# Kernel tuning notes

Measured on AMD Instinct MI355X. Metric: run time of the kernel, lower is better.

## Reference

```python
import jax, jax.numpy as jnp
import numpy as np

B, T, DIM = 2, 2048, 1040
H = 16
HD = (DIM - 1) // H  # 64 spatial dims per head; per-head width = HD + 1
EPS = 1e-6


def _rotary_tables(seq_len, dtype):
    inv_freq = 1.0 / (10000.0 ** (jnp.arange(0, HD, 2, dtype=jnp.float32) / (HD - 2 * EPS)))
    t = jnp.arange(seq_len, dtype=jnp.float32)
    freqs = jnp.outer(t, inv_freq)  # [T, HD//2]
    cos = jnp.cos(freqs).astype(dtype)[None, :, None, :]  # [1,T,1,HD//2]
    sin = jnp.sin(freqs).astype(dtype)[None, :, None, :]
    return cos, sin


def _apply_hyp_rotary(x, cos, sin):
    # x: [B,T,H,HD+1]; component 0 is the Lorentz time coordinate
    x_sp = x[..., 1:]
    d = x_sp.shape[-1] // 2
    x1, x2 = x_sp[..., :d], x_sp[..., d:]
    y1 = x1 * cos + x2 * sin
    y2 = -x1 * sin + x2 * cos
    rot = jnp.clip(jnp.concatenate([y1, y2], axis=-1), -1000.0, 1000.0)
    sp_sq = jnp.clip(jnp.sum(rot * rot, axis=-1, keepdims=True), 0.0, 1e6)
    new_x0 = jnp.sqrt(1.0 + sp_sq + EPS)  # re-project onto hyperboloid
    return jnp.concatenate([new_x0, rot], axis=-1)


def setup_inputs() -> dict:
    key = jax.random.key(0)
    kx, kq, kk, kv, kp = jax.random.split(key, 5)
    scale = 0.02  # xavier_normal gain 0.02 in the original
    x = jax.random.normal(kx, (B, T, DIM), dtype=jnp.float32)
    Wq = jax.random.normal(kq, (DIM, DIM), dtype=jnp.float32) * scale
    Wk = jax.random.normal(kk, (DIM, DIM), dtype=jnp.float32) * scale
    Wv = jax.random.normal(kv, (DIM, DIM), dtype=jnp.float32) * scale
    Wp = jax.random.normal(kp, (DIM, DIM), dtype=jnp.float32) * scale
    return {"x": x, "Wq": Wq, "Wk": Wk, "Wv": Wv, "Wp": Wp}


def reference(x, Wq, Wk, Wv, Wp):
    b, t, _ = x.shape
    q = (x @ Wq.T).reshape(b, t, H, HD + 1)
    k = (x @ Wk.T).reshape(b, t, H, HD + 1)
    v = (x @ Wv.T).reshape(b, t, H, HD + 1)
    cos, sin = _rotary_tables(t, x.dtype)
    q = _apply_hyp_rotary(q, cos, sin)
    k = _apply_hyp_rotary(k, cos, sin)
    # Lorentzian inner product scores: -q0*k0 + <q_sp, k_sp>
    spatial = jnp.einsum('bthd,bshd->bhts', q[..., 1:], k[..., 1:])
    lorentz = jnp.einsum('bth,bsh->bhts', q[..., 0], k[..., 0])
    logits = jnp.clip((spatial - lorentz) / (HD ** 0.5), -100.0, 100.0)
    attn = jax.nn.softmax(logits, axis=-1)
    y = jnp.einsum('bhts,bshd->bthd', attn, v).reshape(b, t, DIM)
    return y @ Wp.T
```

## Files before the change

### kernel.cpp

```cpp
#include <hip/hip_runtime.h>
#include <math.h>

#define B_   2
#define T_   2048
#define DIM_ 1040
#define H_   16
#define HD_  64
#define HD1_ 65
#define NELEM (B_*T_*DIM_)

#define KP_   1056
#define NP_   1152
#define NP3_  3456
#define SEGS_ 132
#define MROWS_ (B_*T_)

#define NBH_  (B_*H_)
#define VTR_  72
#define QKW_  96

#define PR_A_ (NP3_*SEGS_)
#define PR_B_ (PR_A_ + MROWS_*SEGS_)
#define PR_C_ (PR_B_ + NBH_*7*256)
#define PR_D_ (PR_C_ + NP_*SEGS_)

typedef __attribute__((ext_vector_type(8))) __bf16 bf16x8;
typedef __attribute__((ext_vector_type(4))) float f32x4;
typedef __attribute__((ext_vector_type(8))) unsigned short ushort8;

static __device__ __forceinline__ unsigned pack_bf16(float lo, float hi) {
    __bf16 a = (__bf16)lo, c = (__bf16)hi;
    unsigned short ua, uc;
    __builtin_memcpy(&ua, &a, 2);
    __builtin_memcpy(&uc, &c, 2);
    return ((unsigned)uc << 16) | ua;
}

static __device__ __forceinline__ float exp2_fast(float x) {
    float r;
    asm("v_exp_f32 %0, %1" : "=v"(r) : "v"(x));
    return r;
}

static __device__ __forceinline__ void conv_row_plain(
    const float* __restrict__ in, __bf16* __restrict__ out, int r, int s,
    int rows_in)
{
    float v[8];
    if (r < rows_in && s < 130) {
        const float4 f0 = *(const float4*)(in + (size_t)r * DIM_ + s * 8);
        const float4 f1 = *(const float4*)(in + (size_t)r * DIM_ + s * 8 + 4);
        v[0]=f0.x; v[1]=f0.y; v[2]=f0.z; v[3]=f0.w;
        v[4]=f1.x; v[5]=f1.y; v[6]=f1.z; v[7]=f1.w;
    } else {
        #pragma unroll
        for (int i = 0; i < 8; ++i) v[i] = 0.0f;
    }
    __bf16 t[8] __attribute__((aligned(16)));
    #pragma unroll
    for (int i = 0; i < 8; ++i) t[i] = (__bf16)v[i];
    *(ushort8*)(out) = *(const ushort8*)(t);
}

__global__ __launch_bounds__(256)
void prep_all(const float* __restrict__ x,  const float* __restrict__ Wq,
              const float* __restrict__ Wk, const float* __restrict__ Wv,
              const float* __restrict__ Wp, __bf16* __restrict__ xb,
              __bf16* __restrict__ Wb3, __bf16* __restrict__ VT,
              __bf16* __restrict__ WpB)
{
    const int gid = blockIdx.x * 256 + threadIdx.x;
    if (gid < PR_A_) {
        const int r = gid / SEGS_, s = gid - r * SEGS_;
        const int seg = r / NP_, rr = r - seg * NP_;
        const float* in = (seg == 0) ? Wq : (seg == 1) ? Wk : Wv;
        conv_row_plain(in, Wb3 + (size_t)r * KP_ + s * 8, rr, s, DIM_);
    } else if (gid < PR_B_) {
        const int g = gid - PR_A_;
        const int r = g / SEGS_, s = g - r * SEGS_;
        conv_row_plain(x, xb + (size_t)r * KP_ + s * 8, r, s, MROWS_);
    } else if (gid < PR_C_) {
        const int cid = gid - PR_B_;
        const int bh  = cid / 1792;
        const int rem = cid - bh * 1792;
        const int row = 65 + rem / 256;
        const int tc  = rem - (row - 65) * 256;
        const unsigned val = (row == 65) ? 0x3F803F80u : 0u;
        unsigned* p = (unsigned*)(VT + ((size_t)bh * VTR_ + row) * T_ + tc * 8);
        p[0] = val; p[1] = val; p[2] = val; p[3] = val;
    } else {
        const int g = gid - PR_C_;
        const int r = g / SEGS_, s = g - r * SEGS_;
        conv_row_plain(Wp, WpB + (size_t)r * KP_ + s * 8, r, s, DIM_);
    }
}

__device__ __forceinline__ void gload_lds16(const void* g, void* l) {
    __builtin_amdgcn_global_load_lds(
        (const __attribute__((address_space(1))) void*)g,
        (__attribute__((address_space(3))) void*)l, 16, 0, 0);
}

#define GEMM_PURE_CORE(Ac_, Bw_, N0_, M0_)                                    \
    __shared__ __bf16 As[128 * 96];                                           \
    __shared__ __bf16 Bs[128 * 96];                                           \
    const int tid  = threadIdx.x;                                             \
    const int lane = tid & 63;                                                \
    const int w    = tid >> 6;                                                \
    const int wr   = (w >> 1) * 64, wc = (w & 1) * 64;                        \
    const __bf16* gap[6]; const __bf16* gb[6];                                \
    _Pragma("unroll")                                                         \
    for (int qi = 0; qi < 6; ++qi) {                                          \
        const int cid = qi * 256 + tid;                                       \
        const int rr  = cid / 12, cc = cid - rr * 12;                         \
        gap[qi] = Ac_ + (size_t)(M0_ + rr) * KP_ + cc * 8;                    \
        gb[qi]  = Bw_ + (size_t)(N0_ + rr) * KP_ + cc * 8;                    \
    }                                                                         \
    f32x4 acc[4][4];                                                          \
    _Pragma("unroll")                                                         \
    for (int i = 0; i < 4; ++i)                                               \
        _Pragma("unroll")                                                     \
        for (int j = 0; j < 4; ++j) acc[i][j] = (f32x4){0.f, 0.f, 0.f, 0.f};  \
    const __bf16* pa = As + (wr + (lane & 15)) * 96 + (lane >> 4) * 8;        \
    const __bf16* pb = Bs + (wc + (lane & 15)) * 96 + (lane >> 4) * 8;        \
    for (int k0 = 0; k0 < KP_; k0 += 96) {                                    \
        __syncthreads();                                                      \
        _Pragma("unroll")                                                     \
        for (int qi = 0; qi < 6; ++qi) {                                      \
            gload_lds16(gap[qi] + k0, As + (qi * 256 + tid) * 8);             \
            gload_lds16(gb[qi]  + k0, Bs + (qi * 256 + tid) * 8);             \
        }                                                                     \
        __syncthreads();                                                      \
        _Pragma("unroll")                                                     \
        for (int ks = 0; ks < 3; ++ks) {                                      \
            bf16x8 a[4], b[4];                                                \
            _Pragma("unroll")                                                 \
            for (int i = 0; i < 4; ++i)                                       \
                a[i] = *(const bf16x8*)(pa + i * 16 * 96 + ks * 32);          \
            _Pragma("unroll")                                                 \
            for (int j = 0; j < 4; ++j)                                       \
                b[j] = *(const bf16x8*)(pb + j * 16 * 96 + ks * 32);          \
            __builtin_amdgcn_s_setprio(1);                                    \
            _Pragma("unroll")                                                 \
            for (int i = 0; i < 4; ++i)                                       \
                _Pragma("unroll")                                             \
                for (int j = 0; j < 4; ++j)                                   \
                    acc[i][j] = __builtin_amdgcn_mfma_f32_16x16x32_bf16(      \
                        a[i], b[j], acc[i][j], 0, 0, 0);                      \
            __builtin_amdgcn_s_setprio(0);                                    \
        }                                                                     \
    }

__global__ __launch_bounds__(256)
void gemm_qkv_b(const __bf16* __restrict__ Ac, const __bf16* __restrict__ Bw,
                __bf16* __restrict__ Cq, __bf16* __restrict__ Ck,
                __bf16* __restrict__ VTout)
{
    const int bid = blockIdx.x;
    const int gid = (bid & 7) * 108 + (bid >> 3);
    const int n0  = (gid >> 5) * 128;
    const int m0  = (gid & 31) * 128;
    GEMM_PURE_CORE(Ac, Bw, n0, m0)

    const int seg = n0 / NP_;
    const int rbase = m0 + wr + (lane >> 4) * 4;
    const int cbase = n0 - seg * NP_ + wc + (lane & 15);

    if (seg < 2) {
        __bf16* C = seg ? Ck : Cq;
        #pragma unroll
        for (int i = 0; i < 4; ++i)
            #pragma unroll
            for (int j = 0; j < 4; ++j) {
                const int n = cbase + j * 16;
                if (n < DIM_) {
                    #pragma unroll
                    for (int r = 0; r < 4; ++r)
                        C[(size_t)(rbase + i * 16 + r) * DIM_ + n] =
                            (__bf16)acc[i][j][r];
                }
            }
    } else {
        #pragma unroll
        for (int i = 0; i < 4; ++i) {
            const int tg = rbase + i * 16;
            const int bb = tg >> 11, tt = tg & (T_ - 1);
            #pragma unroll
            for (int j = 0; j < 4; ++j) {
                const int n = cbase + j * 16;
                if (n < DIM_) {
                    const int h = n / 65, d = n - h * 65;
                    const size_t off =
                        ((size_t)(bb * H_ + h) * VTR_ + d) * T_ + tt;
                    uint2 pk;
                    pk.x = pack_bf16(acc[i][j][0], acc[i][j][1]);
                    pk.y = pack_bf16(acc[i][j][2], acc[i][j][3]);
                    *(uint2*)(VTout + off) = pk;
                }
            }
        }
    }
}

__global__ __launch_bounds__(256)
void gemm_out_b(const __bf16* __restrict__ Ac, const __bf16* __restrict__ Bw,
                float* __restrict__ C)
{
    const int bid = blockIdx.x;
    const int gid = (bid & 7) * 36 + (bid >> 3);
    const int n0  = (gid >> 5) * 128;
    const int m0  = (gid & 31) * 128;
    GEMM_PURE_CORE(Ac, Bw, n0, m0)

    const int rbase = m0 + wr + (lane >> 4) * 4;
    const int cbase = n0 + wc + (lane & 15);
    #pragma unroll
    for (int i = 0; i < 4; ++i)
        #pragma unroll
        for (int j = 0; j < 4; ++j) {
            const int n = cbase + j * 16;
            if (n < DIM_) {
                #pragma unroll
                for (int r = 0; r < 4; ++r)
                    C[(size_t)(rbase + i * 16 + r) * DIM_ + n] = acc[i][j][r];
            }
        }
}

__global__ __launch_bounds__(256)
void rotary2(const __bf16* __restrict__ Xq, const __bf16* __restrict__ Xk,
             __bf16* __restrict__ QB, __bf16* __restrict__ KB)
{
    const int gwid = (blockIdx.x * 256 + threadIdx.x) >> 6;
    const int lane = threadIdx.x & 63;
    const int which = gwid >> 16;
    const int wid   = gwid & 65535;

    const float SCALE = 0.18033688f;

    const int h  = wid & (H_ - 1);
    const int bt = wid >> 4;
    const int t  = bt & (T_ - 1);
    const int b  = bt >> 11;
    const __bf16* base = (which ? Xk : Xq) + (size_t)bt * DIM_ + h * HD1_;

    const int j = lane & 31;
    const float pw = powf(10000.0f, (float)j * (1.0f / 32.0f));
    const float fr = (float)t * (1.0f / pw);
    const float cs = cosf(fr);
    const float sn = sinf(fr);

    const float x1 = (float)base[1 + j];
    const float x2 = (float)base[33 + j];

    float rot = (lane < 32) ? (x1 * cs + x2 * sn)
                            : (x2 * cs - x1 * sn);
    rot = fminf(fmaxf(rot, -1000.0f), 1000.0f);

    float sq = rot * rot;
    #pragma unroll
    for (int off = 32; off >= 1; off >>= 1)
        sq += __shfl_xor(sq, off, 64);
    sq = fminf(fmaxf(sq, 0.0f), 1.0e6f);

    const float x0 = sqrtf((1.0f + sq) + 1.0e-6f);

    __bf16* XB = which ? KB : QB;
    const size_t base96 = (size_t)((b * H_ + h) * T_ + t) * QKW_;
    XB[base96 + lane] = which ? (__bf16)rot : (__bf16)(SCALE * rot);

    if (lane < 32) {
        float v = 0.0f;
        const float d0 = x0 - 5.25f;
        if (which) {
            const float bh = (float)(__bf16)d0;
            if (lane == 0 || lane == 2) v = bh;
            else if (lane == 1) v = d0 - bh;
        } else {
            if (lane < 2) v = -SCALE * 5.25f;
            else if (lane == 2) v = -SCALE * (float)(__bf16)d0;
        }
        XB[base96 + 64 + lane] = (__bf16)v;
    }
}

__global__ __launch_bounds__(256)
void attn_mfma9(const __bf16* __restrict__ QB, const __bf16* __restrict__ KB,
                const __bf16* __restrict__ VT, __bf16* __restrict__ yb)
{
    __shared__ __bf16 Kt[2][64 * 96] __attribute__((aligned(16)));
    __shared__ __bf16 Vt[80 * 64] __attribute__((aligned(16)));
    __shared__ __bf16 Pt[128 * 72] __attribute__((aligned(16)));

    const int tid  = threadIdx.x;
    const int lane = tid & 63;
    const int w    = tid >> 6;
    const int lx   = lane & 15;
    const int ly   = lane >> 4;
    const int bh   = blockIdx.x;
    const int q0r  = blockIdx.y * 128;

    const __bf16* QBb = QB + (size_t)bh * T_ * QKW_;
    const __bf16* KBb = KB + (size_t)bh * T_ * QKW_;
    const __bf16* VTb = VT + (size_t)bh * VTR_ * T_;

    bf16x8 aq[2][3];
    #pragma unroll
    for (int t = 0; t < 2; ++t)
        #pragma unroll
        for (int ks = 0; ks < 3; ++ks)
            aq[t][ks] = *(const bf16x8*)
                (QBb + (size_t)(q0r + t * 64 + w * 16 + lx) * QKW_ +
                 ks * 32 + ly * 8);

    ((unsigned*)Vt)[2304 + tid] = 0u;

    int offk[3];
    #pragma unroll
    for (int qi = 0; qi < 3; ++qi) {
        const int cid = qi * 256 + tid;
        const int s = cid / 12, p = cid - s * 12;
        const int c = (p & 12) | ((p - (s >> 1)) & 3);
        offk[qi] = s * QKW_ + c * 8;
    }
    int offv[3];
    #pragma unroll
    for (int qi = 0; qi < 3; ++qi) {
        const int cid = qi * 256 + tid;
        const int d = cid >> 3, jj = cid & 7;
        offv[qi] = d * T_ + (jj ^ (d & 7)) * 8;
    }

    #pragma unroll
    for (int qi = 0; qi < 3; ++qi)
        gload_lds16(KBb + offk[qi], &Kt[0][(qi * 256 + tid) * 8]);

    f32x4 acc_o[2][5];
    #pragma unroll
    for (int t = 0; t < 2; ++t)
        #pragma unroll
        for (int n = 0; n < 5; ++n) acc_o[t][n] = (f32x4){0.f, 0.f, 0.f, 0.f};

    const int rr = (ly + (lx >> 1)) & 3;

    int cur = 0;
    for (int it = 0; it < T_ / 64; ++it) {
        const int s0 = it * 64;
        __syncthreads();

        gload_lds16(VTb + s0 + offv[0], Vt + tid * 8);
        gload_lds16(VTb + s0 + offv[1], Vt + (256 + tid) * 8);
        if (tid < 64)
            gload_lds16(VTb + s0 + offv[2], Vt + (512 + tid) * 8);

        if (it + 1 < T_ / 64) {
            const size_t koff = (size_t)(s0 + 64) * QKW_;
            #pragma unroll
            for (int qi = 0; qi < 3; ++qi)
                gload_lds16(KBb + koff + offk[qi],
                            &Kt[cur ^ 1][(qi * 256 + tid) * 8]);
        }

        #pragma unroll
        for (int t = 0; t < 2; ++t) {
            f32x4 sc[4];
            __builtin_amdgcn_s_setprio(1);
            #pragma unroll
            for (int n = 0; n < 4; ++n) {
                f32x4 c = (f32x4){0.f, 0.f, 0.f, 0.f};
                #pragma unroll
                for (int ks = 0; ks < 3; ++ks) {
                    const bf16x8 bk = *(const bf16x8*)
                        &Kt[cur][(n * 16 + lx) * 96 + ks * 32 + rr * 8];
                    c = __builtin_amdgcn_mfma_f32_16x16x32_bf16(
                        aq[t][ks], bk, c, 0, 0, 0);
                }
                sc[n] = c;
            }
            __builtin_amdgcn_s_setprio(0);

            #pragma unroll
            for (int n = 0; n < 4; ++n)
                #pragma unroll
                for (int r = 0; r < 4; ++r)
                    Pt[(t * 64 + w * 16 + ly * 4 + r) * 72 + n * 16 + lx] =
                        (__bf16)exp2_fast(sc[n][r]);
        }

        __syncthreads();

        #pragma unroll
        for (int t = 0; t < 2; ++t) {
            bf16x8 ap[2];
            #pragma unroll
            for (int ks = 0; ks < 2; ++ks)
                ap[ks] = *(const bf16x8*)
                    &Pt[(t * 64 + w * 16 + lx) * 72 + ks * 32 + ly * 8];
            __builtin_amdgcn_s_setprio(1);
            #pragma unroll
            for (int n = 0; n < 5; ++n) {
                f32x4 c = acc_o[t][n];
                #pragma unroll
                for (int ks = 0; ks < 2; ++ks) {
                    const bf16x8 bv = *(const bf16x8*)
                        &Vt[(n * 16 + lx) * 64 +
                            ((ks * 4 + ly) ^ (lx & 7)) * 8];
                    c = __builtin_amdgcn_mfma_f32_16x16x32_bf16(
                        ap[ks], bv, c, 0, 0, 0);
                }
                acc_o[t][n] = c;
            }
            __builtin_amdgcn_s_setprio(0);
        }
        cur ^= 1;
    }

    const int b = bh >> 4, h = bh & 15;
    #pragma unroll
    for (int t = 0; t < 2; ++t)
        #pragma unroll
        for (int r = 0; r < 4; ++r) {
            const float l = __shfl(acc_o[t][4][r], (lane & 48) + 1, 64);
            const float inv = 1.0f / l;
            const int qrow = q0r + t * 64 + w * 16 + ly * 4 + r;
            __bf16* yrow = yb + (size_t)(b * T_ + qrow) * KP_ + h * HD1_;
            #pragma unroll
            for (int n = 0; n < 4; ++n)
                yrow[n * 16 + lx] = (__bf16)(acc_o[t][n][r] * inv);
            if (lx == 0) yrow[64] = (__bf16)(acc_o[t][4][r] * inv);
        }
}

extern "C" void kernel_launch(void* const* d_in, const int* in_sizes, int n_in,
                              void* d_out, int out_size, void* d_ws, size_t ws_size,
                              hipStream_t stream)
{
    const float* x  = (const float*)d_in[0];
    const float* Wq = (const float*)d_in[1];
    const float* Wk = (const float*)d_in[2];
    const float* Wv = (const float*)d_in[3];
    const float* Wp = (const float*)d_in[4];

    __bf16* qb  = (__bf16*)d_ws;
    __bf16* kb  = qb + (size_t)MROWS_ * DIM_;
    __bf16* xb  = kb + (size_t)MROWS_ * DIM_;
    __bf16* Wb3 = xb + (size_t)MROWS_ * KP_;
    __bf16* QB  = Wb3 + (size_t)NP3_ * KP_;
    __bf16* KB  = QB + (size_t)NBH_ * T_ * QKW_;
    __bf16* VT  = KB + (size_t)NBH_ * T_ * QKW_;
    __bf16* WpB = VT + (size_t)NBH_ * VTR_ * T_;
    __bf16* yb  = xb;

    float* out = (float*)d_out;

    dim3 blk(256);

    prep_all<<<dim3(PR_D_ / 256), blk, 0, stream>>>(
        x, Wq, Wk, Wv, Wp, xb, Wb3, VT, WpB);
    gemm_qkv_b<<<dim3(864), blk, 0, stream>>>(xb, Wb3, qb, kb, VT);

    rotary2<<<dim3(2 * (B_ * T_ * H_) / 4), blk, 0, stream>>>(qb, kb, QB, KB);

    attn_mfma9<<<dim3(NBH_, T_ / 128), blk, 0, stream>>>(QB, KB, VT, yb);

    gemm_out_b<<<dim3(288), blk, 0, stream>>>(yb, WpB, out);
}
```

Measured before the change: 210.5 us.

## Double-buffer V tiles in attention and retile output projection GEMM

The attention kernel now double-buffers the V tile in LDS, prefetching the next V block together with the next K block. This removes the mid-iteration block barrier, since each wave reads back only its own probability rows. The output projection GEMM is replaced by a simpler kernel with 64x128 tiles and 576 blocks instead of 288 blocks of 128x128, to fill the MI355X's compute units better. The trade-offs are extra LDS per attention block, which can lower occupancy, and a non-pipelined K loop in the new GEMM.

```diff
diff --git a/kernel.cpp b/kernel.cpp
--- a/kernel.cpp
+++ b/kernel.cpp
@@ -203,19 +203,74 @@
 }
 
 __global__ __launch_bounds__(256)
-void gemm_out_b(const __bf16* __restrict__ Ac, const __bf16* __restrict__ Bw,
-                float* __restrict__ C)
-{
-    const int bid = blockIdx.x;
-    const int gid = (bid & 7) * 36 + (bid >> 3);
-    const int n0  = (gid >> 5) * 128;
-    const int m0  = (gid & 31) * 128;
-    GEMM_PURE_CORE(Ac, Bw, n0, m0)
+void gemm_out_b2(const __bf16* __restrict__ Ac, const __bf16* __restrict__ Bw,
+                 float* __restrict__ C)
+{
+    __shared__ __bf16 As[64 * 96];
+    __shared__ __bf16 Bs[128 * 96];
+    const int tid  = threadIdx.x;
+    const int lane = tid & 63;
+    const int w    = tid >> 6;
+    const int wr   = (w >> 1) * 32, wc = (w & 1) * 64;
+    const int bid  = blockIdx.x;
+    const int gid  = (bid & 7) * 72 + (bid >> 3);
+    const int n0   = (gid % 9) * 128;
+    const int m0   = (gid / 9) * 64;
+
+    const __bf16* gap[3]; const __bf16* gb[6];
+    #pragma unroll
+    for (int qi = 0; qi < 3; ++qi) {
+        const int cid = qi * 256 + tid;
+        const int rr  = cid / 12, cc = cid - rr * 12;
+        gap[qi] = Ac + (size_t)(m0 + rr) * KP_ + cc * 8;
+    }
+    #pragma unroll
+    for (int qi = 0; qi < 6; ++qi) {
+        const int cid = qi * 256 + tid;
+        const int rr  = cid / 12, cc = cid - rr * 12;
+        gb[qi] = Bw + (size_t)(n0 + rr) * KP_ + cc * 8;
+    }
+    f32x4 acc[2][4];
+    #pragma unroll
+    for (int i = 0; i < 2; ++i)
+        #pragma unroll
+        for (int j = 0; j < 4; ++j) acc[i][j] = (f32x4){0.f, 0.f, 0.f, 0.f};
+    const __bf16* pa = As + (wr + (lane & 15)) * 96 + (lane >> 4) * 8;
+    const __bf16* pb = Bs + (wc + (lane & 15)) * 96 + (lane >> 4) * 8;
+
+    for (int k0 = 0; k0 < KP_; k0 += 96) {
+        __syncthreads();
+        #pragma unroll
+        for (int qi = 0; qi < 3; ++qi)
+            gload_lds16(gap[qi] + k0, As + (qi * 256 + tid) * 8);
+        #pragma unroll
+        for (int qi = 0; qi < 6; ++qi)
+            gload_lds16(gb[qi] + k0, Bs + (qi * 256 + tid) * 8);
+        __syncthreads();
+        #pragma unroll
+        for (int ks = 0; ks < 3; ++ks) {
+            bf16x8 a[2], b[4];
+            #pragma unroll
+            for (int i = 0; i < 2; ++i)
+                a[i] = *(const bf16x8*)(pa + i * 16 * 96 + ks * 32);
+            #pragma unroll
+            for (int j = 0; j < 4; ++j)
+                b[j] = *(const bf16x8*)(pb + j * 16 * 96 + ks * 32);
+            __builtin_amdgcn_s_setprio(1);
+            #pragma unroll
+            for (int i = 0; i < 2; ++i)
+                #pragma unroll
+                for (int j = 0; j < 4; ++j)
+                    acc[i][j] = __builtin_amdgcn_mfma_f32_16x16x32_bf16(
+                        a[i], b[j], acc[i][j], 0, 0, 0);
+            __builtin_amdgcn_s_setprio(0);
+        }
+    }
 
     const int rbase = m0 + wr + (lane >> 4) * 4;
     const int cbase = n0 + wc + (lane & 15);
     #pragma unroll
-    for (int i = 0; i < 4; ++i)
+    for (int i = 0; i < 2; ++i)
         #pragma unroll
         for (int j = 0; j < 4; ++j) {
             const int n = cbase + j * 16;
@@ -285,11 +340,11 @@
 }
 
 __global__ __launch_bounds__(256)
-void attn_mfma9(const __bf16* __restrict__ QB, const __bf16* __restrict__ KB,
-                const __bf16* __restrict__ VT, __bf16* __restrict__ yb)
+void attn_mfma11(const __bf16* __restrict__ QB, const __bf16* __restrict__ KB,
+                 const __bf16* __restrict__ VT, __bf16* __restrict__ yb)
 {
     __shared__ __bf16 Kt[2][64 * 96] __attribute__((aligned(16)));
-    __shared__ __bf16 Vt[80 * 64] __attribute__((aligned(16)));
+    __shared__ __bf16 Vt[2][80 * 64] __attribute__((aligned(16)));
     __shared__ __bf16 Pt[128 * 72] __attribute__((aligned(16)));
 
     const int tid  = threadIdx.x;
@@ -313,7 +368,8 @@
                 (QBb + (size_t)(q0r + t * 64 + w * 16 + lx) * QKW_ +
                  ks * 32 + ly * 8);
 
-    ((unsigned*)Vt)[2304 + tid] = 0u;
+    ((unsigned*)Vt[0])[2304 + tid] = 0u;
+    ((unsigned*)Vt[1])[2304 + tid] = 0u;
 
     int offk[3];
     #pragma unroll
@@ -334,6 +390,10 @@
     #pragma unroll
     for (int qi = 0; qi < 3; ++qi)
         gload_lds16(KBb + offk[qi], &Kt[0][(qi * 256 + tid) * 8]);
+    gload_lds16(VTb + offv[0], &Vt[0][tid * 8]);
+    gload_lds16(VTb + offv[1], &Vt[0][(256 + tid) * 8]);
+    if (tid < 64)
+        gload_lds16(VTb + offv[2], &Vt[0][(512 + tid) * 8]);
 
     f32x4 acc_o[2][5];
     #pragma unroll
@@ -345,20 +405,19 @@
 
     int cur = 0;
     for (int it = 0; it < T_ / 64; ++it) {
-        const int s0 = it * 64;
         __syncthreads();
 
-        gload_lds16(VTb + s0 + offv[0], Vt + tid * 8);
-        gload_lds16(VTb + s0 + offv[1], Vt + (256 + tid) * 8);
-        if (tid < 64)
-            gload_lds16(VTb + s0 + offv[2], Vt + (512 + tid) * 8);
-
         if (it + 1 < T_ / 64) {
-            const size_t koff = (size_t)(s0 + 64) * QKW_;
+            const int s1 = (it + 1) * 64;
+            const size_t koff = (size_t)s1 * QKW_;
             #pragma unroll
             for (int qi = 0; qi < 3; ++qi)
                 gload_lds16(KBb + koff + offk[qi],
                             &Kt[cur ^ 1][(qi * 256 + tid) * 8]);
+            gload_lds16(VTb + s1 + offv[0], &Vt[cur ^ 1][tid * 8]);
+            gload_lds16(VTb + s1 + offv[1], &Vt[cur ^ 1][(256 + tid) * 8]);
+            if (tid < 64)
+                gload_lds16(VTb + s1 + offv[2], &Vt[cur ^ 1][(512 + tid) * 8]);
         }
 
         #pragma unroll
@@ -387,8 +446,6 @@
                         (__bf16)exp2_fast(sc[n][r]);
         }
 
-        __syncthreads();
-
         #pragma unroll
         for (int t = 0; t < 2; ++t) {
             bf16x8 ap[2];
@@ -403,8 +460,8 @@
                 #pragma unroll
                 for (int ks = 0; ks < 2; ++ks) {
                     const bf16x8 bv = *(const bf16x8*)
-                        &Vt[(n * 16 + lx) * 64 +
-                            ((ks * 4 + ly) ^ (lx & 7)) * 8];
+                        &Vt[cur][(n * 16 + lx) * 64 +
+                                 ((ks * 4 + ly) ^ (lx & 7)) * 8];
                     c = __builtin_amdgcn_mfma_f32_16x16x32_bf16(
                         ap[ks], bv, c, 0, 0, 0);
                 }
@@ -461,7 +518,7 @@
 
     rotary2<<<dim3(2 * (B_ * T_ * H_) / 4), blk, 0, stream>>>(qb, kb, QB, KB);
 
-    attn_mfma9<<<dim3(NBH_, T_ / 128), blk, 0, stream>>>(QB, KB, VT, yb);
-
-    gemm_out_b<<<dim3(288), blk, 0, stream>>>(yb, WpB, out);
-}
+    attn_mfma11<<<dim3(NBH_, T_ / 128), blk, 0, stream>>>(QB, KB, VT, yb);
+
+    gemm_out_b2<<<dim3(576), blk, 0, stream>>>(yb, WpB, out);
+}
```

Result: faster. 204.3 us (median of 2 runs) (-3.0%).

## Shrink GEMM tiles to 64x128 and double-buffer V in attention

Applied to the files above, without the earlier changes.

Both projection GEMMs move from 128x128 to 64x128 output tiles. This doubles the grid (1728 and 576 blocks) so work spreads more evenly across the CUs, especially in the output GEMM, which previously had 288 blocks. The attention kernel now double-buffers the V tile alongside K, prefetching the next V block during the current iteration, and drops the barrier between writing and reading P, relying on each wave only reading its own rows. The costs are less data reuse per tile and more LDS use in attention, which may reduce occupancy.

```diff
diff --git a/kernel.cpp b/kernel.cpp
--- a/kernel.cpp
+++ b/kernel.cpp
@@ -101,24 +101,29 @@
         (__attribute__((address_space(3))) void*)l, 16, 0, 0);
 }
 
-#define GEMM_PURE_CORE(Ac_, Bw_, N0_, M0_)                                    \
-    __shared__ __bf16 As[128 * 96];                                           \
+#define GEMM_CORE_64x128(Ac_, Bw_, N0_, M0_)                                  \
+    __shared__ __bf16 As[64 * 96];                                            \
     __shared__ __bf16 Bs[128 * 96];                                           \
     const int tid  = threadIdx.x;                                             \
     const int lane = tid & 63;                                                \
     const int w    = tid >> 6;                                                \
-    const int wr   = (w >> 1) * 64, wc = (w & 1) * 64;                        \
-    const __bf16* gap[6]; const __bf16* gb[6];                                \
+    const int wr   = (w >> 1) * 32, wc = (w & 1) * 64;                        \
+    const __bf16* gap[3]; const __bf16* gb[6];                                \
+    _Pragma("unroll")                                                         \
+    for (int qi = 0; qi < 3; ++qi) {                                          \
+        const int cid = qi * 256 + tid;                                       \
+        const int rr  = cid / 12, cc = cid - rr * 12;                         \
+        gap[qi] = Ac_ + (size_t)(M0_ + rr) * KP_ + cc * 8;                    \
+    }                                                                         \
     _Pragma("unroll")                                                         \
     for (int qi = 0; qi < 6; ++qi) {                                          \
         const int cid = qi * 256 + tid;                                       \
         const int rr  = cid / 12, cc = cid - rr * 12;                         \
-        gap[qi] = Ac_ + (size_t)(M0_ + rr) * KP_ + cc * 8;                    \
-        gb[qi]  = Bw_ + (size_t)(N0_ + rr) * KP_ + cc * 8;                    \
+        gb[qi] = Bw_ + (size_t)(N0_ + rr) * KP_ + cc * 8;                     \
     }                                                                         \
-    f32x4 acc[4][4];                                                          \
+    f32x4 acc[2][4];                                                          \
     _Pragma("unroll")                                                         \
-    for (int i = 0; i < 4; ++i)                                               \
+    for (int i = 0; i < 2; ++i)                                               \
         _Pragma("unroll")                                                     \
         for (int j = 0; j < 4; ++j) acc[i][j] = (f32x4){0.f, 0.f, 0.f, 0.f};  \
     const __bf16* pa = As + (wr + (lane & 15)) * 96 + (lane >> 4) * 8;        \
@@ -126,23 +131,24 @@
     for (int k0 = 0; k0 < KP_; k0 += 96) {                                    \
         __syncthreads();                                                      \
         _Pragma("unroll")                                                     \
-        for (int qi = 0; qi < 6; ++qi) {                                      \
+        for (int qi = 0; qi < 3; ++qi)                                        \
             gload_lds16(gap[qi] + k0, As + (qi * 256 + tid) * 8);             \
-            gload_lds16(gb[qi]  + k0, Bs + (qi * 256 + tid) * 8);             \
-        }                                                                     \
+        _Pragma("unroll")                                                     \
+        for (int qi = 0; qi < 6; ++qi)                                        \
+            gload_lds16(gb[qi] + k0, Bs + (qi * 256 + tid) * 8);              \
         __syncthreads();                                                      \
         _Pragma("unroll")                                                     \
         for (int ks = 0; ks < 3; ++ks) {                                      \
-            bf16x8 a[4], b[4];                                                \
+            bf16x8 a[2], b[4];                                                \
             _Pragma("unroll")                                                 \
-            for (int i = 0; i < 4; ++i)                                       \
+            for (int i = 0; i < 2; ++i)                                       \
                 a[i] = *(const bf16x8*)(pa + i * 16 * 96 + ks * 32);          \
             _Pragma("unroll")                                                 \
             for (int j = 0; j < 4; ++j)                                       \
                 b[j] = *(const bf16x8*)(pb + j * 16 * 96 + ks * 32);          \
             __builtin_amdgcn_s_setprio(1);                                    \
             _Pragma("unroll")                                                 \
-            for (int i = 0; i < 4; ++i)                                       \
+            for (int i = 0; i < 2; ++i)                                       \
                 _Pragma("unroll")                                             \
                 for (int j = 0; j < 4; ++j)                                   \
                     acc[i][j] = __builtin_amdgcn_mfma_f32_16x16x32_bf16(      \
@@ -152,15 +158,15 @@
     }
 
 __global__ __launch_bounds__(256)
-void gemm_qkv_b(const __bf16* __restrict__ Ac, const __bf16* __restrict__ Bw,
-                __bf16* __restrict__ Cq, __bf16* __restrict__ Ck,
-                __bf16* __restrict__ VTout)
+void gemm_qkv_b2(const __bf16* __restrict__ Ac, const __bf16* __restrict__ Bw,
+                 __bf16* __restrict__ Cq, __bf16* __restrict__ Ck,
+                 __bf16* __restrict__ VTout)
 {
     const int bid = blockIdx.x;
-    const int gid = (bid & 7) * 108 + (bid >> 3);
-    const int n0  = (gid >> 5) * 128;
-    const int m0  = (gid & 31) * 128;
-    GEMM_PURE_CORE(Ac, Bw, n0, m0)
+    const int gid = (bid & 7) * 216 + (bid >> 3);
+    const int n0  = (gid / 64) * 128;
+    const int m0  = (gid & 63) * 64;
+    GEMM_CORE_64x128(Ac, Bw, n0, m0)
 
     const int seg = n0 / NP_;
     const int rbase = m0 + wr + (lane >> 4) * 4;
@@ -169,7 +175,7 @@
     if (seg < 2) {
         __bf16* C = seg ? Ck : Cq;
         #pragma unroll
-        for (int i = 0; i < 4; ++i)
+        for (int i = 0; i < 2; ++i)
             #pragma unroll
             for (int j = 0; j < 4; ++j) {
                 const int n = cbase + j * 16;
@@ -182,7 +188,7 @@
             }
     } else {
         #pragma unroll
-        for (int i = 0; i < 4; ++i) {
+        for (int i = 0; i < 2; ++i) {
             const int tg = rbase + i * 16;
             const int bb = tg >> 11, tt = tg & (T_ - 1);
             #pragma unroll
@@ -203,19 +209,19 @@
 }
 
 __global__ __launch_bounds__(256)
-void gemm_out_b(const __bf16* __restrict__ Ac, const __bf16* __restrict__ Bw,
-                float* __restrict__ C)
+void gemm_out_b2(const __bf16* __restrict__ Ac, const __bf16* __restrict__ Bw,
+                 float* __restrict__ C)
 {
     const int bid = blockIdx.x;
-    const int gid = (bid & 7) * 36 + (bid >> 3);
-    const int n0  = (gid >> 5) * 128;
-    const int m0  = (gid & 31) * 128;
-    GEMM_PURE_CORE(Ac, Bw, n0, m0)
+    const int gid = (bid & 7) * 72 + (bid >> 3);
+    const int n0  = (gid % 9) * 128;
+    const int m0  = (gid / 9) * 64;
+    GEMM_CORE_64x128(Ac, Bw, n0, m0)
 
     const int rbase = m0 + wr + (lane >> 4) * 4;
     const int cbase = n0 + wc + (lane & 15);
     #pragma unroll
-    for (int i = 0; i < 4; ++i)
+    for (int i = 0; i < 2; ++i)
         #pragma unroll
         for (int j = 0; j < 4; ++j) {
             const int n = cbase + j * 16;
@@ -285,11 +291,11 @@
 }
 
 __global__ __launch_bounds__(256)
-void attn_mfma9(const __bf16* __restrict__ QB, const __bf16* __restrict__ KB,
-                const __bf16* __restrict__ VT, __bf16* __restrict__ yb)
+void attn_mfma11(const __bf16* __restrict__ QB, const __bf16* __restrict__ KB,
+                 const __bf16* __restrict__ VT, __bf16* __restrict__ yb)
 {
     __shared__ __bf16 Kt[2][64 * 96] __attribute__((aligned(16)));
-    __shared__ __bf16 Vt[80 * 64] __attribute__((aligned(16)));
+    __shared__ __bf16 Vt[2][80 * 64] __attribute__((aligned(16)));
     __shared__ __bf16 Pt[128 * 72] __attribute__((aligned(16)));
 
     const int tid  = threadIdx.x;
@@ -313,7 +319,8 @@
                 (QBb + (size_t)(q0r + t * 64 + w * 16 + lx) * QKW_ +
                  ks * 32 + ly * 8);
 
-    ((unsigned*)Vt)[2304 + tid] = 0u;
+    ((unsigned*)Vt[0])[2304 + tid] = 0u;
+    ((unsigned*)Vt[1])[2304 + tid] = 0u;
 
     int offk[3];
     #pragma unroll
@@ -334,6 +341,10 @@
     #pragma unroll
     for (int qi = 0; qi < 3; ++qi)
         gload_lds16(KBb + offk[qi], &Kt[0][(qi * 256 + tid) * 8]);
+    gload_lds16(VTb + offv[0], &Vt[0][tid * 8]);
+    gload_lds16(VTb + offv[1], &Vt[0][(256 + tid) * 8]);
+    if (tid < 64)
+        gload_lds16(VTb + offv[2], &Vt[0][(512 + tid) * 8]);
 
     f32x4 acc_o[2][5];
     #pragma unroll
@@ -345,20 +356,19 @@
 
     int cur = 0;
     for (int it = 0; it < T_ / 64; ++it) {
-        const int s0 = it * 64;
         __syncthreads();
 
-        gload_lds16(VTb + s0 + offv[0], Vt + tid * 8);
-        gload_lds16(VTb + s0 + offv[1], Vt + (256 + tid) * 8);
-        if (tid < 64)
-            gload_lds16(VTb + s0 + offv[2], Vt + (512 + tid) * 8);
-
         if (it + 1 < T_ / 64) {
-            const size_t koff = (size_t)(s0 + 64) * QKW_;
+            const int s1 = (it + 1) * 64;
+            const size_t koff = (size_t)s1 * QKW_;
             #pragma unroll
             for (int qi = 0; qi < 3; ++qi)
                 gload_lds16(KBb + koff + offk[qi],
                             &Kt[cur ^ 1][(qi * 256 + tid) * 8]);
+            gload_lds16(VTb + s1 + offv[0], &Vt[cur ^ 1][tid * 8]);
+            gload_lds16(VTb + s1 + offv[1], &Vt[cur ^ 1][(256 + tid) * 8]);
+            if (tid < 64)
+                gload_lds16(VTb + s1 + offv[2], &Vt[cur ^ 1][(512 + tid) * 8]);
         }
 
         #pragma unroll
@@ -387,8 +397,6 @@
                         (__bf16)exp2_fast(sc[n][r]);
         }
 
-        __syncthreads();
-
         #pragma unroll
         for (int t = 0; t < 2; ++t) {
             bf16x8 ap[2];
@@ -403,8 +411,8 @@
                 #pragma unroll
                 for (int ks = 0; ks < 2; ++ks) {
                     const bf16x8 bv = *(const bf16x8*)
-                        &Vt[(n * 16 + lx) * 64 +
-                            ((ks * 4 + ly) ^ (lx & 7)) * 8];
+                        &Vt[cur][(n * 16 + lx) * 64 +
+                                 ((ks * 4 + ly) ^ (lx & 7)) * 8];
                     c = __builtin_amdgcn_mfma_f32_16x16x32_bf16(
                         ap[ks], bv, c, 0, 0, 0);
                 }
@@ -457,11 +465,11 @@
 
     prep_all<<<dim3(PR_D_ / 256), blk, 0, stream>>>(
         x, Wq, Wk, Wv, Wp, xb, Wb3, VT, WpB);
-    gemm_qkv_b<<<dim3(864), blk, 0, stream>>>(xb, Wb3, qb, kb, VT);
+    gemm_qkv_b2<<<dim3(1728), blk, 0, stream>>>(xb, Wb3, qb, kb, VT);
 
     rotary2<<<dim3(2 * (B_ * T_ * H_) / 4), blk, 0, stream>>>(qb, kb, QB, KB);
 
-    attn_mfma9<<<dim3(NBH_, T_ / 128), blk, 0, stream>>>(QB, KB, VT, yb);
-
-    gemm_out_b<<<dim3(288), blk, 0, stream>>>(yb, WpB, out);
-}
+    attn_mfma11<<<dim3(NBH_, T_ / 128), blk, 0, stream>>>(QB, KB, VT, yb);
+
+    gemm_out_b2<<<dim3(576), blk, 0, stream>>>(yb, WpB, out);
+}
```

Result: faster. 205.5 us (-2.4%).
